# Kernel optimization log

Hardware: AMD Instinct MI355X
Metric: run time of the kernel (lower is better)

Reference implementation:

```python
import jax, jax.numpy as jnp
import numpy as np

N = 6144       # num nodes
F_IN = 256     # in_channels
HID = 64       # hidden
OUT = 64       # out_channels
E = 196608     # num edges (avg degree 32)
ALPHA = 0.8
EPS = 1e-6     # prob clamp (stand-in for torch clamp_probs tiny)
BN_EPS = 1e-5


def setup_inputs() -> dict:
    key = jax.random.key(0)
    ks = jax.random.split(key, 6)
    x = jax.random.normal(ks[0], (N, F_IN), jnp.float32)
    edge_index = jax.random.randint(ks[1], (2, E), 0, N, dtype=jnp.int64)
    W1 = jax.random.normal(ks[2], (F_IN, HID), jnp.float32) / np.float32(np.sqrt(F_IN))
    b1 = jnp.zeros((HID,), jnp.float32)
    W2 = jax.random.normal(ks[3], (HID, OUT), jnp.float32) / np.float32(np.sqrt(HID))
    b2 = jnp.zeros((OUT,), jnp.float32)
    gamma = jnp.ones((HID,), jnp.float32)
    beta = jnp.zeros((HID,), jnp.float32)
    prelu_a = jnp.full((1,), 0.25, jnp.float32)
    u = jax.random.uniform(ks[4], (N, N), jnp.float32, minval=1e-6, maxval=1.0 - 1e-6)
    return dict(x=x, edge_index=edge_index, W1=W1, b1=b1, W2=W2, b2=b2,
                gamma=gamma, beta=beta, prelu_a=prelu_a, u=u)


def _gcn_edge(x, src, dst, W, b, n):
    # PyG GCNConv: add self-loops, D^-1/2 (A+I) D^-1/2 (x W) + b
    h = x @ W
    loop = jnp.arange(n, dtype=src.dtype)
    src2 = jnp.concatenate([src, loop])
    dst2 = jnp.concatenate([dst, loop])
    deg = jax.ops.segment_sum(jnp.ones_like(src2, h.dtype), dst2, num_segments=n)
    dinv = jax.lax.rsqrt(deg)  # deg >= 1 due to self-loops
    norm = dinv[src2] * dinv[dst2]
    out = jax.ops.segment_sum(h[src2] * norm[:, None], dst2, num_segments=n)
    return out + b


def reference(x, edge_index, W1, b1, W2, b2, gamma, beta, prelu_a, u):
    n = x.shape[0]
    src, dst = edge_index[0], edge_index[1]

    # --- sample(alpha=0.8, x, edge_index) ---
    h = _gcn_edge(x, src, dst, W1, b1, n)                      # conv1 on original graph
    adj_orig = jnp.zeros((n, n), h.dtype).at[src, dst].set(1.0)  # directed scatter, as in the loop
    adj_logits = h @ h.T                                        # [N, N]
    edge_probs = ALPHA * (adj_logits / jnp.max(adj_logits)) + (1.0 - ALPHA) * adj_orig
    edge_probs = jnp.maximum(edge_probs, 0.0)                   # where(p<0, 0, p)
    p = jnp.clip(edge_probs, EPS, 1.0 - EPS)
    logits = jnp.log(p) - jnp.log1p(-p)
    noise = jnp.log(u) - jnp.log1p(-u)                          # logistic noise
    soft = jax.nn.sigmoid(logits + noise)                       # RelaxedBernoulli, temperature=1
    st = soft + jax.lax.stop_gradient(jnp.round(soft) - soft)   # straight-through hard sample
    a = jnp.triu(st, 1)
    a = a + a.T
    eye = jnp.eye(n, dtype=a.dtype)
    adj_sampled = a + eye                                       # fill_diagonal_(1) (triu(1) zeroed diag)

    # --- main conv stack on sampled graph (nonzero -> edge list -> GCNConv adds self-loops again) ---
    A = adj_sampled + eye                                       # diag weight becomes 2, faithful to PyG
    dinv = jax.lax.rsqrt(A.sum(axis=1))
    An = dinv[:, None] * A * dinv[None, :]
    x1 = An @ (x @ W1) + b1                                     # conv 0
    z = jnp.where(x1 >= 0, x1, prelu_a * x1)                    # PReLU
    mean = x1.mean(axis=0)
    var = x1.var(axis=0)                                        # biased, training-mode BN
    xb = gamma * (x1 - mean) * jax.lax.rsqrt(var + BN_EPS) + beta
    xr = jax.nn.relu(xb)                                        # dropout p=0 is a no-op
    x2 = An @ (xr @ W2) + b2                                    # conv 1
    return (x2, z, adj_sampled, adj_logits, adj_orig)
```

## Files before the change

### kernel.cpp

```cpp
#include <hip/hip_runtime.h>
#include <math.h>

#define NN 6144
#define FIN 256
#define HID 64
#define NW 96
typedef unsigned long long u64;


__global__ __launch_bounds__(256) void k_hxw(const float* __restrict__ x,
                                             const float* __restrict__ W1,
                                             double* __restrict__ hxw) {
  int t = blockIdx.x * 256 + threadIdx.x;
  int i = t >> 6, c = t & 63;
  const float* xr = x + (size_t)i * FIN;
  double a = 0.0;
#pragma unroll 8
  for (int k = 0; k < FIN; ++k)
    a = fma((double)xr[k], (double)W1[k * HID + c], a);
  hxw[t] = a;
}

__global__ __launch_bounds__(256) void k_edges(const int* __restrict__ ei, int E,
                                               int* __restrict__ deg,
                                               float* __restrict__ adjO,
                                               u64* __restrict__ bitO) {
  int e = blockIdx.x * 256 + threadIdx.x;
  if (e >= E) return;
  int s = ei[e], d = ei[E + e];
  atomicAdd(&deg[d], 1);
  adjO[(size_t)s * NN + d] = 1.0f;
  atomicOr(&bitO[(size_t)s * NW + (d >> 6)], 1ull << (d & 63));
}

__global__ __launch_bounds__(256) void k_dinv(const int* __restrict__ deg,
                                              double* __restrict__ dinv) {
  int i = blockIdx.x * 256 + threadIdx.x;
  if (i < NN) dinv[i] = 1.0 / sqrt((double)(deg[i] + 1));
}

__global__ __launch_bounds__(256) void k_agg(const int* __restrict__ ei, int E,
                                             const double* __restrict__ hxw,
                                             const double* __restrict__ dinv,
                                             double* __restrict__ hagg) {
  int t = blockIdx.x * 256 + threadIdx.x;
  if (t >= E * HID) return;
  int e = t >> 6, c = t & 63;
  int s = ei[e], d = ei[E + e];
  atomicAdd(&hagg[(size_t)d * HID + c], hxw[(size_t)s * HID + c] * (dinv[s] * dinv[d]));
}

__global__ __launch_bounds__(256) void k_selfbias(const double* __restrict__ hxw,
                                                  const double* __restrict__ dinv,
                                                  const float* __restrict__ b1,
                                                  double* __restrict__ hagg) {
  int t = blockIdx.x * 256 + threadIdx.x;
  int i = t >> 6, c = t & 63;
  hagg[t] += hxw[t] * dinv[i] * dinv[i] + (double)b1[c];
}

__global__ __launch_bounds__(256) void k_lmax(const double* __restrict__ h,
                                              u64* __restrict__ lmax) {
  __shared__ double red[256];
  int i = blockIdx.x * 256 + threadIdx.x;
  const double* hr = h + (size_t)i * HID;
  double s = 0.0;
  for (int c = 0; c < HID; ++c) s = fma(hr[c], hr[c], s);
  red[threadIdx.x] = s;
  __syncthreads();
  for (int w = 128; w > 0; w >>= 1) {
    if (threadIdx.x < w) {
      double o = red[threadIdx.x + w];
      if (o > red[threadIdx.x]) red[threadIdx.x] = o;
    }
    __syncthreads();
  }
  if (threadIdx.x == 0)
    atomicMax(lmax, (u64)__double_as_longlong(red[0]));
}

__global__ __launch_bounds__(256) void k_tile(const double* __restrict__ h,
                                              const u64* __restrict__ lmaxp,
                                              const float* __restrict__ u,
                                              const u64* __restrict__ bitO,
                                              float* __restrict__ adjL,
                                              float* __restrict__ adjS,
                                              u64* __restrict__ bitS) {
  int I = blockIdx.y, J = blockIdx.x;
  if (J < I) return;
  __shared__ __align__(16) double smem[64 * 68];
  double* As = smem;
  double* Bs = smem + 64 * 33;
  float* Ls = (float*)smem;
  float* Ss = ((float*)smem) + 64 * 68;
  int t = threadIdx.x;
  int tx = t & 15, ty = t >> 4;
  double acc[4][4];
#pragma unroll
  for (int p = 0; p < 4; ++p)
#pragma unroll
    for (int q = 0; q < 4; ++q) acc[p][q] = 0.0;
  const double* hI = h + (size_t)I * 64 * HID;
  const double* hJ = h + (size_t)J * 64 * HID;
  for (int k0 = 0; k0 < 64; k0 += 32) {
    __syncthreads();
    for (int idx = t; idx < 2048; idx += 256) {
      int r = idx >> 5, k = idx & 31;
      As[r * 33 + k] = hI[r * 64 + k0 + k];
      Bs[r * 33 + k] = hJ[r * 64 + k0 + k];
    }
    __syncthreads();
#pragma unroll 8
    for (int k = 0; k < 32; ++k) {
      double a0 = As[ty * 33 + k], a1 = As[(ty + 16) * 33 + k];
      double a2 = As[(ty + 32) * 33 + k], a3 = As[(ty + 48) * 33 + k];
      double c0 = Bs[tx * 33 + k], c1 = Bs[(tx + 16) * 33 + k];
      double c2 = Bs[(tx + 32) * 33 + k], c3 = Bs[(tx + 48) * 33 + k];
      acc[0][0] = fma(a0, c0, acc[0][0]); acc[0][1] = fma(a0, c1, acc[0][1]);
      acc[0][2] = fma(a0, c2, acc[0][2]); acc[0][3] = fma(a0, c3, acc[0][3]);
      acc[1][0] = fma(a1, c0, acc[1][0]); acc[1][1] = fma(a1, c1, acc[1][1]);
      acc[1][2] = fma(a1, c2, acc[1][2]); acc[1][3] = fma(a1, c3, acc[1][3]);
      acc[2][0] = fma(a2, c0, acc[2][0]); acc[2][1] = fma(a2, c1, acc[2][1]);
      acc[2][2] = fma(a2, c2, acc[2][2]); acc[2][3] = fma(a2, c3, acc[2][3]);
      acc[3][0] = fma(a3, c0, acc[3][0]); acc[3][1] = fma(a3, c1, acc[3][1]);
      acc[3][2] = fma(a3, c2, acc[3][2]); acc[3][3] = fma(a3, c3, acc[3][3]);
    }
  }
  __syncthreads();
  double Lmax = __longlong_as_double((long long)(*lmaxp));
  bool diag = (I == J);
#pragma unroll
  for (int p = 0; p < 4; ++p) {
    int r = ty + 16 * p;
    int gi = I * 64 + r;
    float sv[4];
#pragma unroll
    for (int q = 0; q < 4; ++q) {
      int c = tx + 16 * q;
      int gj = J * 64 + c;
      double L = acc[p][q];
      float lf = (float)L;
      adjL[(size_t)gi * NN + gj] = lf;
      float stv;
      if (diag && r == c) {
        stv = 1.0f;
      } else {
        int ga = gi < gj ? gi : gj, gb = gi < gj ? gj : gi;
        size_t ab = (size_t)ga * NN + gb;
        double uu = (double)u[ab];
        double ao = (double)(int)((bitO[(size_t)ga * NW + (gb >> 6)] >> (gb & 63)) & 1ull);
        double ep = 0.8 * (L / Lmax) + 0.2 * ao;
        if (ep < 0.0) ep = 0.0;
        double pl = ep;
        if (pl < 1e-6) pl = 1e-6;
        double hi = 1.0 - 1e-6;
        if (pl > hi) pl = hi;
        stv = (pl > 1.0 - uu) ? 1.0f : 0.0f;
      }
      sv[q] = stv;
      adjS[(size_t)gi * NN + gj] = stv;
      if (!diag) {
        Ls[c * 68 + r] = lf;
        Ss[c * 68 + r] = stv;
      }
    }
    u64 word = 0;
#pragma unroll
    for (int q = 0; q < 4; ++q) {
      u64 m = __ballot(sv[q] > 0.5f);
      word |= ((m >> ((ty & 3) * 16)) & 0xFFFFull) << (16 * q);
    }
    if (tx == 0) bitS[(size_t)gi * NW + J] = word;
  }
  if (!diag) {
    __syncthreads();
    for (int i4 = t; i4 < 1024; i4 += 256) {
      int a = i4 >> 4, b4 = (i4 & 15) << 2;
      size_t off = (size_t)(J * 64 + a) * NN + (I * 64 + b4);
      *(float4*)(adjL + off) = *(const float4*)&Ls[a * 68 + b4];
      *(float4*)(adjS + off) = *(const float4*)&Ss[a * 68 + b4];
    }
    for (int k2 = 0; k2 < 16; ++k2) {
      int idx = t + (k2 << 8);
      int a = idx >> 6, b = idx & 63;
      u64 m = __ballot(Ss[a * 68 + b] > 0.5f);
      if ((t & 63) == 0) bitS[(size_t)(J * 64 + a) * NW + I] = m;
    }
  }
}

__global__ __launch_bounds__(256) void k_rowsumB(const u64* __restrict__ bitS,
                                                 double* __restrict__ dinv2) {
  int i = blockIdx.x * 256 + threadIdx.x;
  const u64* row = bitS + (size_t)i * NW;
  int cnt = 0;
#pragma unroll
  for (int wdx = 0; wdx < NW; ++wdx) cnt += __popcll(row[wdx]);
  dinv2[i] = 1.0 / sqrt((double)(cnt + 1));
}

__global__ __launch_bounds__(256) void k_gscale(const double* __restrict__ hv,
                                                const double* __restrict__ dinv2,
                                                float* __restrict__ g) {
  int t = blockIdx.x * 256 + threadIdx.x;
  int j = t >> 6;
  g[t] = (float)(dinv2[j] * hv[t]);
}

__global__ __launch_bounds__(256) void k_anmm(const u64* __restrict__ bitS,
                                              const float* __restrict__ g,
                                              float* __restrict__ accb) {
  int I = blockIdx.x;
  int s = blockIdx.y;
  __shared__ __align__(16) float as[64 * 65];
  __shared__ __align__(16) float gs[64 * 64];
  int t = threadIdx.x, tx = t & 15, ty = t >> 4;
  float acc[4][4];
#pragma unroll
  for (int p = 0; p < 4; ++p)
#pragma unroll
    for (int q = 0; q < 4; ++q) acc[p][q] = 0.0f;
  for (int Jt = s * 12; Jt < (s + 1) * 12; ++Jt) {
    __syncthreads();
    for (int i4 = t; i4 < 1024; i4 += 256) {
      int r = i4 >> 4, c4 = (i4 & 15) << 2;
      *(float4*)&gs[r * 64 + c4] = *(const float4*)&g[(size_t)(Jt * 64 + r) * HID + c4];
    }
    for (int idx = t; idx < 4096; idx += 256) {
      int r = idx >> 6, cc = idx & 63;
      u64 w = bitS[(size_t)(I * 64 + r) * NW + Jt];
      as[r * 65 + cc] = (float)((w >> cc) & 1ull);
    }
    __syncthreads();
#pragma unroll 4
    for (int j = 0; j < 64; ++j) {
      float4 cv = *(const float4*)&gs[j * 64 + (tx << 2)];
      float a0 = as[ty * 65 + j], a1 = as[(ty + 16) * 65 + j];
      float a2 = as[(ty + 32) * 65 + j], a3 = as[(ty + 48) * 65 + j];
      acc[0][0] = fmaf(a0, cv.x, acc[0][0]); acc[0][1] = fmaf(a0, cv.y, acc[0][1]);
      acc[0][2] = fmaf(a0, cv.z, acc[0][2]); acc[0][3] = fmaf(a0, cv.w, acc[0][3]);
      acc[1][0] = fmaf(a1, cv.x, acc[1][0]); acc[1][1] = fmaf(a1, cv.y, acc[1][1]);
      acc[1][2] = fmaf(a1, cv.z, acc[1][2]); acc[1][3] = fmaf(a1, cv.w, acc[1][3]);
      acc[2][0] = fmaf(a2, cv.x, acc[2][0]); acc[2][1] = fmaf(a2, cv.y, acc[2][1]);
      acc[2][2] = fmaf(a2, cv.z, acc[2][2]); acc[2][3] = fmaf(a2, cv.w, acc[2][3]);
      acc[3][0] = fmaf(a3, cv.x, acc[3][0]); acc[3][1] = fmaf(a3, cv.y, acc[3][1]);
      acc[3][2] = fmaf(a3, cv.z, acc[3][2]); acc[3][3] = fmaf(a3, cv.w, acc[3][3]);
    }
  }
  float* out = accb + (size_t)s * NN * HID;
#pragma unroll
  for (int p = 0; p < 4; ++p) {
    float4 v = make_float4(acc[p][0], acc[p][1], acc[p][2], acc[p][3]);
    *(float4*)&out[(size_t)(I * 64 + ty + 16 * p) * HID + (tx << 2)] = v;
  }
}

__global__ __launch_bounds__(256) void k_ep1(const float* __restrict__ accb,
                                             const float* __restrict__ g,
                                             const double* __restrict__ dinv2,
                                             const float* __restrict__ b1,
                                             const float* __restrict__ prelu,
                                             float* __restrict__ x1,
                                             float* __restrict__ zout) {
  int t = blockIdx.x * 256 + threadIdx.x;
  int i = t >> 6, c = t & 63;
  double ss = 0.0;
  for (int s = 0; s < 8; ++s) ss += (double)accb[(size_t)s * NN * HID + t];
  float v = (float)(dinv2[i] * (ss + (double)g[t])) + b1[c];
  x1[t] = v;
  float pa = prelu[0];
  zout[t] = v >= 0.0f ? v : pa * v;
}

__global__ __launch_bounds__(256) void k_bnstats(const float* __restrict__ x1,
                                                 double* __restrict__ meanv,
                                                 double* __restrict__ istd) {
  __shared__ double r1[256], r2[256];
  int c = blockIdx.x;
  double s1 = 0.0, s2 = 0.0;
  for (int i = threadIdx.x; i < NN; i += 256) {
    double v = (double)x1[(size_t)i * HID + c];
    s1 += v;
    s2 += v * v;
  }
  r1[threadIdx.x] = s1;
  r2[threadIdx.x] = s2;
  __syncthreads();
  for (int w = 128; w > 0; w >>= 1) {
    if (threadIdx.x < w) {
      r1[threadIdx.x] += r1[threadIdx.x + w];
      r2[threadIdx.x] += r2[threadIdx.x + w];
    }
    __syncthreads();
  }
  if (threadIdx.x == 0) {
    double m = r1[0] / (double)NN;
    double var = r2[0] / (double)NN - m * m;
    meanv[c] = m;
    istd[c] = 1.0 / sqrt(var + 1e-5);
  }
}

__global__ __launch_bounds__(256) void k_xr(const float* __restrict__ x1,
                                            const double* __restrict__ meanv,
                                            const double* __restrict__ istd,
                                            const float* __restrict__ gamma,
                                            const float* __restrict__ beta,
                                            float* __restrict__ xr) {
  int t = blockIdx.x * 256 + threadIdx.x;
  int c = t & 63;
  float v = gamma[c] * (float)(((double)x1[t] - meanv[c]) * istd[c]) + beta[c];
  xr[t] = v > 0.0f ? v : 0.0f;
}

__global__ __launch_bounds__(256) void k_y_g2(const float* __restrict__ xr,
                                              const float* __restrict__ W2,
                                              const double* __restrict__ dinv2,
                                              float* __restrict__ g2) {
  int t = blockIdx.x * 256 + threadIdx.x;
  int j = t >> 6, c = t & 63;
  const float* xrow = xr + (size_t)j * HID;
  float a = 0.0f;
#pragma unroll 8
  for (int k = 0; k < HID; ++k) a = fmaf(xrow[k], W2[k * HID + c], a);
  g2[t] = (float)(dinv2[j] * (double)a);
}

__global__ __launch_bounds__(256) void k_ep2(const float* __restrict__ accb,
                                             const float* __restrict__ g2,
                                             const double* __restrict__ dinv2,
                                             const float* __restrict__ b2p,
                                             float* __restrict__ x2out) {
  int t = blockIdx.x * 256 + threadIdx.x;
  int i = t >> 6, c = t & 63;
  double ss = 0.0;
  for (int s = 0; s < 8; ++s) ss += (double)accb[(size_t)s * NN * HID + t];
  x2out[t] = (float)(dinv2[i] * (ss + (double)g2[t])) + b2p[c];
}

extern "C" void kernel_launch(void* const* d_in, const int* in_sizes, int n_in,
                              void* d_out, int out_size, void* d_ws, size_t ws_size,
                              hipStream_t stream) {
  const float* x = (const float*)d_in[0];
  const int* ei = (const int*)d_in[1];
  const float* W1 = (const float*)d_in[2];
  const float* b1 = (const float*)d_in[3];
  const float* W2 = (const float*)d_in[4];
  const float* b2 = (const float*)d_in[5];
  const float* gamma = (const float*)d_in[6];
  const float* beta = (const float*)d_in[7];
  const float* prelu = (const float*)d_in[8];
  const float* u = (const float*)d_in[9];
  int E = in_sizes[1] / 2;

  float* out = (float*)d_out;
  float* o_x2 = out;
  float* o_z = out + (size_t)NN * HID;
  float* o_adjS = out + (size_t)2 * NN * HID;
  float* o_adjL = o_adjS + (size_t)NN * NN;
  float* o_adjO = o_adjL + (size_t)NN * NN;

  char* w = (char*)d_ws;
  double* hxw = (double*)w;
  double* hagg = (double*)(w + 3145728);
  double* dinv = (double*)(w + 6291456);
  int* deg = (int*)(w + 6340608);
  float* accb = (float*)w;
  double* dinv2 = (double*)(w + 12582912);
  u64* lmax = (u64*)(w + 12632064);
  double* meanv = (double*)(w + 12632128);
  double* istd = (double*)(w + 12632640);
  float* x1 = (float*)(w + 12633152);
  float* gg = (float*)(w + 14206016);
  float* xr = (float*)(w + 15778880);
  float* g2 = (float*)(w + 17351744);
  u64* bitO = (u64*)(w + 12633152);
  u64* bitS = (u64*)(w + 18924608);

  hipMemsetAsync(deg, 0, NN * sizeof(int), stream);
  hipMemsetAsync(hagg, 0, (size_t)NN * HID * sizeof(double), stream);
  hipMemsetAsync(lmax, 0, sizeof(u64), stream);
  hipMemsetAsync(bitO, 0, (size_t)NN * NW * sizeof(u64), stream);
  hipMemsetAsync(o_adjO, 0, (size_t)NN * NN * sizeof(float), stream);

  k_hxw<<<NN * HID / 256, 256, 0, stream>>>(x, W1, hxw);
  k_edges<<<(E + 255) / 256, 256, 0, stream>>>(ei, E, deg, o_adjO, bitO);
  k_dinv<<<NN / 256, 256, 0, stream>>>(deg, dinv);
  k_agg<<<(E * HID + 255) / 256, 256, 0, stream>>>(ei, E, hxw, dinv, hagg);
  k_selfbias<<<NN * HID / 256, 256, 0, stream>>>(hxw, dinv, b1, hagg);
  k_lmax<<<NN / 256, 256, 0, stream>>>(hagg, lmax);
  dim3 gt(96, 96);
  k_tile<<<gt, 256, 0, stream>>>(hagg, lmax, u, bitO, o_adjL, o_adjS, bitS);
  k_rowsumB<<<NN / 256, 256, 0, stream>>>(bitS, dinv2);
  k_gscale<<<NN * HID / 256, 256, 0, stream>>>(hxw, dinv2, gg);
  dim3 ga(96, 8);
  k_anmm<<<ga, 256, 0, stream>>>(bitS, gg, accb);
  k_ep1<<<NN * HID / 256, 256, 0, stream>>>(accb, gg, dinv2, b1, prelu, x1, o_z);
  k_bnstats<<<HID, 256, 0, stream>>>(x1, meanv, istd);
  k_xr<<<NN * HID / 256, 256, 0, stream>>>(x1, meanv, istd, gamma, beta, xr);
  k_y_g2<<<NN * HID / 256, 256, 0, stream>>>(xr, W2, dinv2, g2);
  k_anmm<<<ga, 256, 0, stream>>>(bitS, g2, accb);
  k_ep2<<<NN * HID / 256, 256, 0, stream>>>(accb, g2, dinv2, b2, o_x2);
}
```

Before: 1.058 ms.

## Write adj_orig in tile kernel, transpose sample bitmask, vectorize LDS loads, fuse BN+W2

The dense adj_orig output is now produced inside the tile kernel from the bitO bitmask, which removes the 151MB memset and the scattered per-edge float stores. The sampled-adjacency bitmask is stored column-block-major (bitT) so that k_anmm and k_rowsumB read it with coalesced accesses. The LDS reads in k_tile and k_anmm are widened to double2/float4 with padded strides. The BN/ReLU and W2 matmul kernels are fused through shared memory. The tile kernel now does extra bitO reads and adj_orig writes.

```diff
diff --git a/kernel.cpp b/kernel.cpp
--- a/kernel.cpp
+++ b/kernel.cpp
@@ -23,13 +23,11 @@
 
 __global__ __launch_bounds__(256) void k_edges(const int* __restrict__ ei, int E,
                                                int* __restrict__ deg,
-                                               float* __restrict__ adjO,
                                                u64* __restrict__ bitO) {
   int e = blockIdx.x * 256 + threadIdx.x;
   if (e >= E) return;
   int s = ei[e], d = ei[E + e];
   atomicAdd(&deg[d], 1);
-  adjO[(size_t)s * NN + d] = 1.0f;
   atomicOr(&bitO[(size_t)s * NW + (d >> 6)], 1ull << (d & 63));
 }
 
@@ -79,18 +77,29 @@
     atomicMax(lmax, (u64)__double_as_longlong(red[0]));
 }
 
+#define FMA16D(A0, A1, A2, A3, C0, C1, C2, C3)                                   \
+  acc[0][0] = fma(A0, C0, acc[0][0]); acc[0][1] = fma(A0, C1, acc[0][1]);        \
+  acc[0][2] = fma(A0, C2, acc[0][2]); acc[0][3] = fma(A0, C3, acc[0][3]);        \
+  acc[1][0] = fma(A1, C0, acc[1][0]); acc[1][1] = fma(A1, C1, acc[1][1]);        \
+  acc[1][2] = fma(A1, C2, acc[1][2]); acc[1][3] = fma(A1, C3, acc[1][3]);        \
+  acc[2][0] = fma(A2, C0, acc[2][0]); acc[2][1] = fma(A2, C1, acc[2][1]);        \
+  acc[2][2] = fma(A2, C2, acc[2][2]); acc[2][3] = fma(A2, C3, acc[2][3]);        \
+  acc[3][0] = fma(A3, C0, acc[3][0]); acc[3][1] = fma(A3, C1, acc[3][1]);        \
+  acc[3][2] = fma(A3, C2, acc[3][2]); acc[3][3] = fma(A3, C3, acc[3][3]);
+
 __global__ __launch_bounds__(256) void k_tile(const double* __restrict__ h,
                                               const u64* __restrict__ lmaxp,
                                               const float* __restrict__ u,
                                               const u64* __restrict__ bitO,
                                               float* __restrict__ adjL,
                                               float* __restrict__ adjS,
-                                              u64* __restrict__ bitS) {
+                                              float* __restrict__ adjO,
+                                              u64* __restrict__ bitT) {
   int I = blockIdx.y, J = blockIdx.x;
   if (J < I) return;
-  __shared__ __align__(16) double smem[64 * 68];
+  __shared__ __align__(16) double smem[2 * 64 * 34];
   double* As = smem;
-  double* Bs = smem + 64 * 33;
+  double* Bs = smem + 64 * 34;
   float* Ls = (float*)smem;
   float* Ss = ((float*)smem) + 64 * 68;
   int t = threadIdx.x;
@@ -104,26 +113,24 @@
   const double* hJ = h + (size_t)J * 64 * HID;
   for (int k0 = 0; k0 < 64; k0 += 32) {
     __syncthreads();
-    for (int idx = t; idx < 2048; idx += 256) {
-      int r = idx >> 5, k = idx & 31;
-      As[r * 33 + k] = hI[r * 64 + k0 + k];
-      Bs[r * 33 + k] = hJ[r * 64 + k0 + k];
+    for (int idx = t; idx < 1024; idx += 256) {
+      int r = idx >> 4, k2 = (idx & 15) << 1;
+      *(double2*)&As[r * 34 + k2] = *(const double2*)&hI[r * 64 + k0 + k2];
+      *(double2*)&Bs[r * 34 + k2] = *(const double2*)&hJ[r * 64 + k0 + k2];
     }
     __syncthreads();
 #pragma unroll 8
-    for (int k = 0; k < 32; ++k) {
-      double a0 = As[ty * 33 + k], a1 = As[(ty + 16) * 33 + k];
-      double a2 = As[(ty + 32) * 33 + k], a3 = As[(ty + 48) * 33 + k];
-      double c0 = Bs[tx * 33 + k], c1 = Bs[(tx + 16) * 33 + k];
-      double c2 = Bs[(tx + 32) * 33 + k], c3 = Bs[(tx + 48) * 33 + k];
-      acc[0][0] = fma(a0, c0, acc[0][0]); acc[0][1] = fma(a0, c1, acc[0][1]);
-      acc[0][2] = fma(a0, c2, acc[0][2]); acc[0][3] = fma(a0, c3, acc[0][3]);
-      acc[1][0] = fma(a1, c0, acc[1][0]); acc[1][1] = fma(a1, c1, acc[1][1]);
-      acc[1][2] = fma(a1, c2, acc[1][2]); acc[1][3] = fma(a1, c3, acc[1][3]);
-      acc[2][0] = fma(a2, c0, acc[2][0]); acc[2][1] = fma(a2, c1, acc[2][1]);
-      acc[2][2] = fma(a2, c2, acc[2][2]); acc[2][3] = fma(a2, c3, acc[2][3]);
-      acc[3][0] = fma(a3, c0, acc[3][0]); acc[3][1] = fma(a3, c1, acc[3][1]);
-      acc[3][2] = fma(a3, c2, acc[3][2]); acc[3][3] = fma(a3, c3, acc[3][3]);
+    for (int k = 0; k < 32; k += 2) {
+      double2 A0 = *(const double2*)&As[ty * 34 + k];
+      double2 A1 = *(const double2*)&As[(ty + 16) * 34 + k];
+      double2 A2 = *(const double2*)&As[(ty + 32) * 34 + k];
+      double2 A3 = *(const double2*)&As[(ty + 48) * 34 + k];
+      double2 C0 = *(const double2*)&Bs[tx * 34 + k];
+      double2 C1 = *(const double2*)&Bs[(tx + 16) * 34 + k];
+      double2 C2 = *(const double2*)&Bs[(tx + 32) * 34 + k];
+      double2 C3 = *(const double2*)&Bs[(tx + 48) * 34 + k];
+      FMA16D(A0.x, A1.x, A2.x, A3.x, C0.x, C1.x, C2.x, C3.x)
+      FMA16D(A0.y, A1.y, A2.y, A3.y, C0.y, C1.y, C2.y, C3.y)
     }
   }
   __syncthreads();
@@ -133,6 +140,7 @@
   for (int p = 0; p < 4; ++p) {
     int r = ty + 16 * p;
     int gi = I * 64 + r;
+    u64 wO = bitO[(size_t)gi * NW + J];
     float sv[4];
 #pragma unroll
     for (int q = 0; q < 4; ++q) {
@@ -141,6 +149,7 @@
       double L = acc[p][q];
       float lf = (float)L;
       adjL[(size_t)gi * NN + gj] = lf;
+      adjO[(size_t)gi * NN + gj] = (float)((wO >> c) & 1ull);
       float stv;
       if (diag && r == c) {
         stv = 1.0f;
@@ -170,32 +179,37 @@
       u64 m = __ballot(sv[q] > 0.5f);
       word |= ((m >> ((ty & 3) * 16)) & 0xFFFFull) << (16 * q);
     }
-    if (tx == 0) bitS[(size_t)gi * NW + J] = word;
+    if (tx == 0) bitT[(size_t)J * NN + gi] = word;
   }
   if (!diag) {
     __syncthreads();
     for (int i4 = t; i4 < 1024; i4 += 256) {
       int a = i4 >> 4, b4 = (i4 & 15) << 2;
-      size_t off = (size_t)(J * 64 + a) * NN + (I * 64 + b4);
+      int grow = J * 64 + a;
+      size_t off = (size_t)grow * NN + (I * 64 + b4);
       *(float4*)(adjL + off) = *(const float4*)&Ls[a * 68 + b4];
       *(float4*)(adjS + off) = *(const float4*)&Ss[a * 68 + b4];
+      u64 wOm = bitO[(size_t)grow * NW + I];
+      *(float4*)(adjO + off) = make_float4((float)((wOm >> b4) & 1ull),
+                                           (float)((wOm >> (b4 + 1)) & 1ull),
+                                           (float)((wOm >> (b4 + 2)) & 1ull),
+                                           (float)((wOm >> (b4 + 3)) & 1ull));
     }
     for (int k2 = 0; k2 < 16; ++k2) {
       int idx = t + (k2 << 8);
       int a = idx >> 6, b = idx & 63;
       u64 m = __ballot(Ss[a * 68 + b] > 0.5f);
-      if ((t & 63) == 0) bitS[(size_t)(J * 64 + a) * NW + I] = m;
-    }
-  }
-}
-
-__global__ __launch_bounds__(256) void k_rowsumB(const u64* __restrict__ bitS,
+      if ((t & 63) == 0) bitT[(size_t)I * NN + (J * 64 + a)] = m;
+    }
+  }
+}
+
+__global__ __launch_bounds__(256) void k_rowsumB(const u64* __restrict__ bitT,
                                                  double* __restrict__ dinv2) {
   int i = blockIdx.x * 256 + threadIdx.x;
-  const u64* row = bitS + (size_t)i * NW;
   int cnt = 0;
 #pragma unroll
-  for (int wdx = 0; wdx < NW; ++wdx) cnt += __popcll(row[wdx]);
+  for (int J = 0; J < NW; ++J) cnt += __popcll(bitT[(size_t)J * NN + i]);
   dinv2[i] = 1.0 / sqrt((double)(cnt + 1));
 }
 
@@ -207,12 +221,22 @@
   g[t] = (float)(dinv2[j] * hv[t]);
 }
 
-__global__ __launch_bounds__(256) void k_anmm(const u64* __restrict__ bitS,
+#define FMA16F(A0, A1, A2, A3, CV)                                                   \
+  acc[0][0] = fmaf(A0, CV.x, acc[0][0]); acc[0][1] = fmaf(A0, CV.y, acc[0][1]);      \
+  acc[0][2] = fmaf(A0, CV.z, acc[0][2]); acc[0][3] = fmaf(A0, CV.w, acc[0][3]);      \
+  acc[1][0] = fmaf(A1, CV.x, acc[1][0]); acc[1][1] = fmaf(A1, CV.y, acc[1][1]);      \
+  acc[1][2] = fmaf(A1, CV.z, acc[1][2]); acc[1][3] = fmaf(A1, CV.w, acc[1][3]);      \
+  acc[2][0] = fmaf(A2, CV.x, acc[2][0]); acc[2][1] = fmaf(A2, CV.y, acc[2][1]);      \
+  acc[2][2] = fmaf(A2, CV.z, acc[2][2]); acc[2][3] = fmaf(A2, CV.w, acc[2][3]);      \
+  acc[3][0] = fmaf(A3, CV.x, acc[3][0]); acc[3][1] = fmaf(A3, CV.y, acc[3][1]);      \
+  acc[3][2] = fmaf(A3, CV.z, acc[3][2]); acc[3][3] = fmaf(A3, CV.w, acc[3][3]);
+
+__global__ __launch_bounds__(256) void k_anmm(const u64* __restrict__ bitT,
                                               const float* __restrict__ g,
                                               float* __restrict__ accb) {
   int I = blockIdx.x;
   int s = blockIdx.y;
-  __shared__ __align__(16) float as[64 * 65];
+  __shared__ __align__(16) float as[64 * 68];
   __shared__ __align__(16) float gs[64 * 64];
   int t = threadIdx.x, tx = t & 15, ty = t >> 4;
   float acc[4][4];
@@ -228,23 +252,24 @@
     }
     for (int idx = t; idx < 4096; idx += 256) {
       int r = idx >> 6, cc = idx & 63;
-      u64 w = bitS[(size_t)(I * 64 + r) * NW + Jt];
-      as[r * 65 + cc] = (float)((w >> cc) & 1ull);
-    }
-    __syncthreads();
-#pragma unroll 4
-    for (int j = 0; j < 64; ++j) {
-      float4 cv = *(const float4*)&gs[j * 64 + (tx << 2)];
-      float a0 = as[ty * 65 + j], a1 = as[(ty + 16) * 65 + j];
-      float a2 = as[(ty + 32) * 65 + j], a3 = as[(ty + 48) * 65 + j];
-      acc[0][0] = fmaf(a0, cv.x, acc[0][0]); acc[0][1] = fmaf(a0, cv.y, acc[0][1]);
-      acc[0][2] = fmaf(a0, cv.z, acc[0][2]); acc[0][3] = fmaf(a0, cv.w, acc[0][3]);
-      acc[1][0] = fmaf(a1, cv.x, acc[1][0]); acc[1][1] = fmaf(a1, cv.y, acc[1][1]);
-      acc[1][2] = fmaf(a1, cv.z, acc[1][2]); acc[1][3] = fmaf(a1, cv.w, acc[1][3]);
-      acc[2][0] = fmaf(a2, cv.x, acc[2][0]); acc[2][1] = fmaf(a2, cv.y, acc[2][1]);
-      acc[2][2] = fmaf(a2, cv.z, acc[2][2]); acc[2][3] = fmaf(a2, cv.w, acc[2][3]);
-      acc[3][0] = fmaf(a3, cv.x, acc[3][0]); acc[3][1] = fmaf(a3, cv.y, acc[3][1]);
-      acc[3][2] = fmaf(a3, cv.z, acc[3][2]); acc[3][3] = fmaf(a3, cv.w, acc[3][3]);
+      u64 w = bitT[(size_t)Jt * NN + I * 64 + r];
+      as[r * 68 + cc] = (float)((w >> cc) & 1ull);
+    }
+    __syncthreads();
+#pragma unroll 2
+    for (int j0 = 0; j0 < 64; j0 += 4) {
+      float4 a0v = *(const float4*)&as[ty * 68 + j0];
+      float4 a1v = *(const float4*)&as[(ty + 16) * 68 + j0];
+      float4 a2v = *(const float4*)&as[(ty + 32) * 68 + j0];
+      float4 a3v = *(const float4*)&as[(ty + 48) * 68 + j0];
+      float4 cv0 = *(const float4*)&gs[j0 * 64 + (tx << 2)];
+      float4 cv1 = *(const float4*)&gs[(j0 + 1) * 64 + (tx << 2)];
+      float4 cv2 = *(const float4*)&gs[(j0 + 2) * 64 + (tx << 2)];
+      float4 cv3 = *(const float4*)&gs[(j0 + 3) * 64 + (tx << 2)];
+      FMA16F(a0v.x, a1v.x, a2v.x, a3v.x, cv0)
+      FMA16F(a0v.y, a1v.y, a2v.y, a3v.y, cv1)
+      FMA16F(a0v.z, a1v.z, a2v.z, a3v.z, cv2)
+      FMA16F(a0v.w, a1v.w, a2v.w, a3v.w, cv3)
     }
   }
   float* out = accb + (size_t)s * NN * HID;
@@ -301,29 +326,27 @@
   }
 }
 
-__global__ __launch_bounds__(256) void k_xr(const float* __restrict__ x1,
-                                            const double* __restrict__ meanv,
-                                            const double* __restrict__ istd,
-                                            const float* __restrict__ gamma,
-                                            const float* __restrict__ beta,
-                                            float* __restrict__ xr) {
-  int t = blockIdx.x * 256 + threadIdx.x;
+__global__ __launch_bounds__(256) void k_xryg2(const float* __restrict__ x1,
+                                               const double* __restrict__ meanv,
+                                               const double* __restrict__ istd,
+                                               const float* __restrict__ gamma,
+                                               const float* __restrict__ beta,
+                                               const float* __restrict__ W2,
+                                               const double* __restrict__ dinv2,
+                                               float* __restrict__ g2) {
+  __shared__ float xs[4 * 64];
+  int t = threadIdx.x;
+  int t2 = blockIdx.x * 256 + t;
   int c = t & 63;
-  float v = gamma[c] * (float)(((double)x1[t] - meanv[c]) * istd[c]) + beta[c];
-  xr[t] = v > 0.0f ? v : 0.0f;
-}
-
-__global__ __launch_bounds__(256) void k_y_g2(const float* __restrict__ xr,
-                                              const float* __restrict__ W2,
-                                              const double* __restrict__ dinv2,
-                                              float* __restrict__ g2) {
-  int t = blockIdx.x * 256 + threadIdx.x;
-  int j = t >> 6, c = t & 63;
-  const float* xrow = xr + (size_t)j * HID;
+  float v = gamma[c] * (float)(((double)x1[t2] - meanv[c]) * istd[c]) + beta[c];
+  xs[t] = v > 0.0f ? v : 0.0f;
+  __syncthreads();
+  const float* xrow = xs + (t >> 6) * 64;
   float a = 0.0f;
 #pragma unroll 8
   for (int k = 0; k < HID; ++k) a = fmaf(xrow[k], W2[k * HID + c], a);
-  g2[t] = (float)(dinv2[j] * (double)a);
+  int j = t2 >> 6;
+  g2[t2] = (float)(dinv2[j] * (double)a);
 }
 
 __global__ __launch_bounds__(256) void k_ep2(const float* __restrict__ accb,
@@ -372,33 +395,30 @@
   double* istd = (double*)(w + 12632640);
   float* x1 = (float*)(w + 12633152);
   float* gg = (float*)(w + 14206016);
-  float* xr = (float*)(w + 15778880);
   float* g2 = (float*)(w + 17351744);
   u64* bitO = (u64*)(w + 12633152);
-  u64* bitS = (u64*)(w + 18924608);
+  u64* bitT = (u64*)(w + 18924608);
 
   hipMemsetAsync(deg, 0, NN * sizeof(int), stream);
   hipMemsetAsync(hagg, 0, (size_t)NN * HID * sizeof(double), stream);
   hipMemsetAsync(lmax, 0, sizeof(u64), stream);
   hipMemsetAsync(bitO, 0, (size_t)NN * NW * sizeof(u64), stream);
-  hipMemsetAsync(o_adjO, 0, (size_t)NN * NN * sizeof(float), stream);
 
   k_hxw<<<NN * HID / 256, 256, 0, stream>>>(x, W1, hxw);
-  k_edges<<<(E + 255) / 256, 256, 0, stream>>>(ei, E, deg, o_adjO, bitO);
+  k_edges<<<(E + 255) / 256, 256, 0, stream>>>(ei, E, deg, bitO);
   k_dinv<<<NN / 256, 256, 0, stream>>>(deg, dinv);
   k_agg<<<(E * HID + 255) / 256, 256, 0, stream>>>(ei, E, hxw, dinv, hagg);
   k_selfbias<<<NN * HID / 256, 256, 0, stream>>>(hxw, dinv, b1, hagg);
   k_lmax<<<NN / 256, 256, 0, stream>>>(hagg, lmax);
   dim3 gt(96, 96);
-  k_tile<<<gt, 256, 0, stream>>>(hagg, lmax, u, bitO, o_adjL, o_adjS, bitS);
-  k_rowsumB<<<NN / 256, 256, 0, stream>>>(bitS, dinv2);
+  k_tile<<<gt, 256, 0, stream>>>(hagg, lmax, u, bitO, o_adjL, o_adjS, o_adjO, bitT);
+  k_rowsumB<<<NN / 256, 256, 0, stream>>>(bitT, dinv2);
   k_gscale<<<NN * HID / 256, 256, 0, stream>>>(hxw, dinv2, gg);
   dim3 ga(96, 8);
-  k_anmm<<<ga, 256, 0, stream>>>(bitS, gg, accb);
+  k_anmm<<<ga, 256, 0, stream>>>(bitT, gg, accb);
   k_ep1<<<NN * HID / 256, 256, 0, stream>>>(accb, gg, dinv2, b1, prelu, x1, o_z);
   k_bnstats<<<HID, 256, 0, stream>>>(x1, meanv, istd);
-  k_xr<<<NN * HID / 256, 256, 0, stream>>>(x1, meanv, istd, gamma, beta, xr);
-  k_y_g2<<<NN * HID / 256, 256, 0, stream>>>(xr, W2, dinv2, g2);
-  k_anmm<<<ga, 256, 0, stream>>>(bitS, g2, accb);
+  k_xryg2<<<NN * HID / 256, 256, 0, stream>>>(x1, meanv, istd, gamma, beta, W2, dinv2, g2);
+  k_anmm<<<ga, 256, 0, stream>>>(bitT, g2, accb);
   k_ep2<<<NN * HID / 256, 256, 0, stream>>>(accb, g2, dinv2, b2, o_x2);
 }
```

Result: no change. 1.046 ms (-1.1%).
